# Kernel tuning notes

Hardware: AMD Instinct MI355X
Metric: run time of the kernel (lower is better)

Reference implementation:

```python
import jax, jax.numpy as jnp
import numpy as np

# UnfoldMatmulFold (VOLO outlook attention): kernel_size=3, strides=2, padding=1,
# final_output_shape=(28,28,768). Only valid config per the layer docstring
# (overlap happens exactly once in the fold).
KS, ST, PAD = 3, 2, 1
H, W, C = 28, 28, 768
NH = 12  # num heads (from attn shape)


def setup_inputs() -> dict:
    key = jax.random.key(0)
    k1, k2 = jax.random.split(key)
    B = 64
    hh, ww = 14, 14  # ceil(H/ST), ceil(W/ST)
    vv = jax.random.normal(k1, (B, H, W, C), dtype=jnp.float32)
    attn = jax.random.normal(k2, (B, hh, ww, NH, KS * KS, KS * KS), dtype=jnp.float32)
    return {"vv": vv, "attn": attn}


def _fold_overlap_1(mm):
    # mm: [B, hh, ww, KS, KS, C].  overlap_pad = 2*ST - KS = 1;
    # hh_pad = ww_pad = [0,0] since ceil(28/2)=14 is even.
    aa = jnp.pad(mm, ((0, 0), (0, 0), (0, 0), (0, 1), (0, 1), (0, 0)))  # [B,hh,ww,4,4,C]
    aa = aa.transpose(0, 1, 3, 2, 4, 5)  # [B, hh, 4, ww, 4, C]

    def pad_overlap(p, sh, sw):
        bb = p[:, sh::2, :, sw::2, :, :]  # [B, hh/2, 4, ww/2, 4, C]
        b0, h1, h2, w1, w2, c = bb.shape
        bb = bb.reshape(b0, h1 * h2, w1 * w2, c)  # [B, 28, 28, C]
        ph = (0, ST) if sh == 0 else (ST, 0)
        pw = (0, ST) if sw == 0 else (ST, 0)
        return jnp.pad(bb, ((0, 0), ph, pw, (0, 0)))  # [B, 30, 30, C]

    cc = (pad_overlap(aa, 0, 0) + pad_overlap(aa, 0, 1)
          + pad_overlap(aa, 1, 0) + pad_overlap(aa, 1, 1))
    return cc[:, PAD:PAD + H, PAD:PAD + W, :]  # [B, H, W, C]


def reference(vv, attn):
    B = vv.shape[0]
    hh, ww, nh = attn.shape[1], attn.shape[2], attn.shape[3]
    dh = C // nh
    # unfold (im2col), padding=SAME-style via explicit pad of KS//2
    pad_vv = jnp.pad(vv, ((0, 0), (PAD, PAD), (PAD, PAD), (0, 0)))
    cols = [pad_vv[:, kh:kh + ST * (hh - 1) + 1:ST, kw:kw + ST * (ww - 1) + 1:ST, :]
            for kh in range(KS) for kw in range(KS)]
    patches = jnp.stack(cols, axis=3)  # [B, hh, ww, KS*KS, C], (kh,kw,C) order like tf.extract_patches
    # matmul: per-location per-head attention over the KS*KS window
    v = patches.reshape(B, hh, ww, KS * KS, nh, dh)
    mm = jnp.einsum('bhwnpq,bhwqnd->bhwpnd', attn, v)  # [B,hh,ww,KS*KS,nh,dh]
    mm = mm.reshape(B, hh, ww, KS, KS, C)
    # fold with overlap-add
    return _fold_overlap_1(mm)
```

## Files before the change

kernel.cpp:

```cpp
#include <hip/hip_runtime.h>
#include <stdint.h>

#define HOUT 28
#define HH   14
#define NHEADS 12
#define CC   768
#define NPIX (HOUT * HOUT)
#define NQ   (HH * HH)
#define AHW  (NHEADS * 81)

template<int IO, int JO>
__device__ __forceinline__ void fma9(float4& acc,
                                     const float* __restrict__ ap,
                                     const float4 (&v)[5][5])
{
    #pragma unroll
    for (int qh = 0; qh < 3; ++qh)
        #pragma unroll
        for (int qw = 0; qw < 3; ++qw) {
            const float  a = ap[3 * qh + qw];
            const float4 u = v[IO + qh][JO + qw];
            acc.x = fmaf(a, u.x, acc.x);
            acc.y = fmaf(a, u.y, acc.y);
            acc.z = fmaf(a, u.z, acc.z);
            acc.w = fmaf(a, u.w, acc.w);
        }
}

__global__ __launch_bounds__(192)
void UnfoldMatmulFold_kernel(const float* __restrict__ vv,
                             const float* __restrict__ attn,
                             float* __restrict__ out)
{
    const unsigned id   = blockIdx.x;
    const unsigned xcd  = id & 7u;
    const unsigned g    = id >> 3;
    const unsigned bgrp = g / 28u;
    const unsigned m    = g - bgrp * 28u;
    const int b   = (int)((bgrp << 3) | xcd);
    const int qy  = (int)(m >> 1);
    const int qx0 = (int)((m & 1u) * 7u);
    const int y0  = qy << 1;

    const int tid = threadIdx.x;
    const int c4  = tid << 2;
    const int n   = tid >> 4;

    const float* vb = vv + (size_t)b * (NPIX * CC) + c4;

    const float* vrow[5];
    bool rowok[5];
    #pragma unroll
    for (int i = 0; i < 5; ++i) {
        const int r  = y0 - 1 + i;
        rowok[i]     = ((unsigned)r < HOUT);
        const int rs = rowok[i] ? r : y0;
        vrow[i] = vb + (size_t)(rs * HOUT) * CC;
    }
    const bool hasY = (qy < 13);

    const float* abq = attn + (size_t)b * (NQ * AHW) + n * 81
                     + (size_t)(qy * HH + qx0) * AHW;

    const size_t obrow = (((size_t)b * HOUT + y0) * HOUT) * CC + c4;

    #pragma unroll 1
    for (int t = 0; t < 7; ++t) {
        const int qx = qx0 + t;
        const int x0 = qx << 1;

        float4 v[5][5];
        #pragma unroll
        for (int i = 0; i < 5; ++i) {
            #pragma unroll
            for (int jj = 0; jj < 5; ++jj) {
                const int cpos = x0 - 1 + jj;
                const int cs   = ((unsigned)cpos < HOUT) ? cpos : x0;
                v[i][jj] = *(const float4*)(vrow[i] + (size_t)cs * CC);
            }
        }
        #pragma unroll
        for (int i = 0; i < 5; ++i) {
            #pragma unroll
            for (int jj = 0; jj < 5; ++jj) {
                const bool cv = (unsigned)(x0 - 1 + jj) < HOUT;
                if (!(rowok[i] && cv)) {
                    v[i][jj].x = 0.f; v[i][jj].y = 0.f;
                    v[i][jj].z = 0.f; v[i][jj].w = 0.f;
                }
            }
        }

        const float* a00 = abq + (size_t)t * AHW;
        const float* a01 = a00 + AHW;
        const float* a10 = a00 + (size_t)HH * AHW;
        const float* a11 = a10 + AHW;
        const bool hasX = (qx < 13);

        const size_t ob = obrow + (size_t)x0 * CC;
        float4 acc;

        acc.x = acc.y = acc.z = acc.w = 0.f;
        fma9<0, 0>(acc, a00 + 4 * 9, v);
        *(float4*)&out[ob] = acc;

        acc.x = acc.y = acc.z = acc.w = 0.f;
        fma9<0, 0>(acc, a00 + 5 * 9, v);
        if (hasX) fma9<0, 2>(acc, a01 + 3 * 9, v);
        *(float4*)&out[ob + CC] = acc;

        acc.x = acc.y = acc.z = acc.w = 0.f;
        fma9<0, 0>(acc, a00 + 7 * 9, v);
        if (hasY) fma9<2, 0>(acc, a10 + 1 * 9, v);
        *(float4*)&out[ob + HOUT * CC] = acc;

        acc.x = acc.y = acc.z = acc.w = 0.f;
        fma9<0, 0>(acc, a00 + 8 * 9, v);
        if (hasX) fma9<0, 2>(acc, a01 + 6 * 9, v);
        if (hasY) fma9<2, 0>(acc, a10 + 2 * 9, v);
        if (hasX && hasY) fma9<2, 2>(acc, a11 + 0 * 9, v);
        *(float4*)&out[ob + (HOUT + 1) * CC] = acc;
    }
}

extern "C" void kernel_launch(void* const* d_in, const int* in_sizes, int n_in,
                              void* d_out, int out_size, void* d_ws, size_t ws_size,
                              hipStream_t stream) {
    const float* vv   = (const float*)d_in[0];
    const float* attn = (const float*)d_in[1];
    float* out        = (float*)d_out;

    const int B = in_sizes[0] / (NPIX * CC);
    dim3 grid((unsigned)(B * 28));
    UnfoldMatmulFold_kernel<<<grid, 192, 0, stream>>>(vv, attn, out);
}
```

Before: 350.9 us.

## Stage attention weights in LDS and process two patch columns per block

Each block now handles one pair of adjacent patch positions with 384 threads, replacing the serial 7-step loop per block. The grid grows to B*98 blocks. The six attention neighbourhoods a block needs are staged cooperatively into shared memory, laid out with padded rows so each thread reads its weights as vector loads. Outputs use nontemporal stores. The aim is more parallelism and fewer redundant scattered global reads of attention weights, at the cost of LDS use, a barrier, and repeated halo loads of vv across blocks.

```diff
diff --git a/kernel.cpp b/kernel.cpp
--- a/kernel.cpp
+++ b/kernel.cpp
@@ -9,118 +9,146 @@
 #define NQ   (HH * HH)
 #define AHW  (NHEADS * 81)
 
+#define ALDS_Q  12
+#define ALDS_P  (9 * ALDS_Q)
+#define ALDS_HW (NHEADS * ALDS_P)
+#define ALDS_TOTAL (6 * ALDS_HW)
+
+typedef float vfloat4 __attribute__((ext_vector_type(4)));
+
 template<int IO, int JO>
-__device__ __forceinline__ void fma9(float4& acc,
-                                     const float* __restrict__ ap,
-                                     const float4 (&v)[5][5])
+__device__ __forceinline__ void fma9L(float4& acc,
+                                      const float* ap,
+                                      const float4 (&v)[5][5])
 {
+    const float4 q0 = *(const float4*)(ap + 0);
+    const float4 q1 = *(const float4*)(ap + 4);
+    const float  a8 = ap[8];
+    const float a[9] = {q0.x, q0.y, q0.z, q0.w, q1.x, q1.y, q1.z, q1.w, a8};
     #pragma unroll
     for (int qh = 0; qh < 3; ++qh)
         #pragma unroll
         for (int qw = 0; qw < 3; ++qw) {
-            const float  a = ap[3 * qh + qw];
-            const float4 u = v[IO + qh][JO + qw];
-            acc.x = fmaf(a, u.x, acc.x);
-            acc.y = fmaf(a, u.y, acc.y);
-            acc.z = fmaf(a, u.z, acc.z);
-            acc.w = fmaf(a, u.w, acc.w);
+            const float  aa = a[qh * 3 + qw];
+            const float4 u  = v[IO + qh][JO + qw];
+            acc.x = fmaf(aa, u.x, acc.x);
+            acc.y = fmaf(aa, u.y, acc.y);
+            acc.z = fmaf(aa, u.z, acc.z);
+            acc.w = fmaf(aa, u.w, acc.w);
         }
 }
 
-__global__ __launch_bounds__(192)
+__global__ __launch_bounds__(384, 3)
 void UnfoldMatmulFold_kernel(const float* __restrict__ vv,
                              const float* __restrict__ attn,
                              float* __restrict__ out)
 {
     const unsigned id   = blockIdx.x;
     const unsigned xcd  = id & 7u;
-    const unsigned g    = id >> 3;
-    const unsigned bgrp = g / 28u;
-    const unsigned m    = g - bgrp * 28u;
+    const unsigned j    = id >> 3;
+    const unsigned bgrp = j / 98u;
+    const unsigned pr   = j - bgrp * 98u;
     const int b   = (int)((bgrp << 3) | xcd);
-    const int qy  = (int)(m >> 1);
-    const int qx0 = (int)((m & 1u) * 7u);
+    const int qy  = (int)(pr / 7u);
+    const int qxp = (int)(pr - (unsigned)qy * 7u);
+    const int w0  = qxp << 1;
     const int y0  = qy << 1;
 
-    const int tid = threadIdx.x;
-    const int c4  = tid << 2;
-    const int n   = tid >> 4;
+    const int tid  = threadIdx.x;
+    const int qloc = tid >= 192;
+    const int t    = tid - (qloc ? 192 : 0);
+    const int c4   = t << 2;
+    const int n    = t >> 4;
+    const int qx   = w0 + qloc;
+    const int x0   = qx << 1;
+
+    __shared__ __align__(16) float att_lds[ALDS_TOTAL];
 
     const float* vb = vv + (size_t)b * (NPIX * CC) + c4;
-
-    const float* vrow[5];
+    float4 v[5][5];
     bool rowok[5];
     #pragma unroll
     for (int i = 0; i < 5; ++i) {
         const int r  = y0 - 1 + i;
         rowok[i]     = ((unsigned)r < HOUT);
         const int rs = rowok[i] ? r : y0;
-        vrow[i] = vb + (size_t)(rs * HOUT) * CC;
+        const float* vrow = vb + (size_t)(rs * HOUT) * CC;
+        #pragma unroll
+        for (int jj = 0; jj < 5; ++jj) {
+            const int cpos = x0 - 1 + jj;
+            const int cs   = ((unsigned)cpos < HOUT) ? cpos : x0;
+            v[i][jj] = *(const float4*)(vrow + (size_t)cs * CC);
+        }
     }
-    const bool hasY = (qy < 13);
 
-    const float* abq = attn + (size_t)b * (NQ * AHW) + n * 81
-                     + (size_t)(qy * HH + qx0) * AHW;
-
-    const size_t obrow = (((size_t)b * HOUT + y0) * HOUT) * CC + c4;
-
-    #pragma unroll 1
-    for (int t = 0; t < 7; ++t) {
-        const int qx = qx0 + t;
-        const int x0 = qx << 1;
-
-        float4 v[5][5];
+    {
+        const float* abase = attn + (size_t)b * (NQ * AHW);
         #pragma unroll
-        for (int i = 0; i < 5; ++i) {
+        for (int c = 0; c < 6; ++c) {
+            const int dy = c / 3, dw = c - dy * 3;
+            int h = qy + dy; if (h > 13) h = 13;
+            int w = w0 + dw; if (w > 13) w = 13;
+            const float* g = abase + (size_t)(h * HH + w) * AHW;
+            float* l = att_lds + c * ALDS_HW;
             #pragma unroll
-            for (int jj = 0; jj < 5; ++jj) {
-                const int cpos = x0 - 1 + jj;
-                const int cs   = ((unsigned)cpos < HOUT) ? cpos : x0;
-                v[i][jj] = *(const float4*)(vrow[i] + (size_t)cs * CC);
-            }
-        }
-        #pragma unroll
-        for (int i = 0; i < 5; ++i) {
-            #pragma unroll
-            for (int jj = 0; jj < 5; ++jj) {
-                const bool cv = (unsigned)(x0 - 1 + jj) < HOUT;
-                if (!(rowok[i] && cv)) {
-                    v[i][jj].x = 0.f; v[i][jj].y = 0.f;
-                    v[i][jj].z = 0.f; v[i][jj].w = 0.f;
+            for (int k = 0; k < 3; ++k) {
+                const int inner = tid + k * 384;
+                if (inner < AHW) {
+                    const int nn = inner / 81;
+                    const int r  = inner - nn * 81;
+                    const int p  = r / 9;
+                    const int q  = r - p * 9;
+                    l[nn * ALDS_P + p * ALDS_Q + q] = g[inner];
                 }
             }
         }
+    }
 
-        const float* a00 = abq + (size_t)t * AHW;
-        const float* a01 = a00 + AHW;
-        const float* a10 = a00 + (size_t)HH * AHW;
-        const float* a11 = a10 + AHW;
-        const bool hasX = (qx < 13);
+    #pragma unroll
+    for (int i = 0; i < 5; ++i) {
+        #pragma unroll
+        for (int jj = 0; jj < 5; ++jj) {
+            const bool cv = (unsigned)(x0 - 1 + jj) < HOUT;
+            if (!(rowok[i] && cv)) {
+                v[i][jj].x = 0.f; v[i][jj].y = 0.f;
+                v[i][jj].z = 0.f; v[i][jj].w = 0.f;
+            }
+        }
+    }
 
-        const size_t ob = obrow + (size_t)x0 * CC;
-        float4 acc;
+    __syncthreads();
 
-        acc.x = acc.y = acc.z = acc.w = 0.f;
-        fma9<0, 0>(acc, a00 + 4 * 9, v);
-        *(float4*)&out[ob] = acc;
+    const float* A00 = att_lds + (0 + qloc    ) * ALDS_HW + n * ALDS_P;
+    const float* A01 = att_lds + (0 + qloc + 1) * ALDS_HW + n * ALDS_P;
+    const float* A10 = att_lds + (3 + qloc    ) * ALDS_HW + n * ALDS_P;
+    const float* A11 = att_lds + (3 + qloc + 1) * ALDS_HW + n * ALDS_P;
 
-        acc.x = acc.y = acc.z = acc.w = 0.f;
-        fma9<0, 0>(acc, a00 + 5 * 9, v);
-        if (hasX) fma9<0, 2>(acc, a01 + 3 * 9, v);
-        *(float4*)&out[ob + CC] = acc;
+    const bool hasX = (qx < 13);
+    const bool hasY = (qy < 13);
 
-        acc.x = acc.y = acc.z = acc.w = 0.f;
-        fma9<0, 0>(acc, a00 + 7 * 9, v);
-        if (hasY) fma9<2, 0>(acc, a10 + 1 * 9, v);
-        *(float4*)&out[ob + HOUT * CC] = acc;
+    const size_t ob = (((size_t)b * HOUT + y0) * HOUT + x0) * CC + c4;
+    float4 acc;
 
-        acc.x = acc.y = acc.z = acc.w = 0.f;
-        fma9<0, 0>(acc, a00 + 8 * 9, v);
-        if (hasX) fma9<0, 2>(acc, a01 + 6 * 9, v);
-        if (hasY) fma9<2, 0>(acc, a10 + 2 * 9, v);
-        if (hasX && hasY) fma9<2, 2>(acc, a11 + 0 * 9, v);
-        *(float4*)&out[ob + (HOUT + 1) * CC] = acc;
-    }
+    acc.x = acc.y = acc.z = acc.w = 0.f;
+    fma9L<0, 0>(acc, A00 + 4 * ALDS_Q, v);
+    __builtin_nontemporal_store(*(vfloat4*)&acc, (vfloat4*)&out[ob]);
+
+    acc.x = acc.y = acc.z = acc.w = 0.f;
+    fma9L<0, 0>(acc, A00 + 5 * ALDS_Q, v);
+    if (hasX) fma9L<0, 2>(acc, A01 + 3 * ALDS_Q, v);
+    __builtin_nontemporal_store(*(vfloat4*)&acc, (vfloat4*)&out[ob + CC]);
+
+    acc.x = acc.y = acc.z = acc.w = 0.f;
+    fma9L<0, 0>(acc, A00 + 7 * ALDS_Q, v);
+    if (hasY) fma9L<2, 0>(acc, A10 + 1 * ALDS_Q, v);
+    __builtin_nontemporal_store(*(vfloat4*)&acc, (vfloat4*)&out[ob + HOUT * CC]);
+
+    acc.x = acc.y = acc.z = acc.w = 0.f;
+    fma9L<0, 0>(acc, A00 + 8 * ALDS_Q, v);
+    if (hasX) fma9L<0, 2>(acc, A01 + 6 * ALDS_Q, v);
+    if (hasY) fma9L<2, 0>(acc, A10 + 2 * ALDS_Q, v);
+    if (hasX && hasY) fma9L<2, 2>(acc, A11 + 0 * ALDS_Q, v);
+    __builtin_nontemporal_store(*(vfloat4*)&acc, (vfloat4*)&out[ob + (HOUT + 1) * CC]);
 }
 
 extern "C" void kernel_launch(void* const* d_in, const int* in_sizes, int n_in,
@@ -131,6 +159,6 @@
     float* out        = (float*)d_out;
 
     const int B = in_sizes[0] / (NPIX * CC);
-    dim3 grid((unsigned)(B * 28));
-    UnfoldMatmulFold_kernel<<<grid, 192, 0, stream>>>(vv, attn, out);
+    dim3 grid((unsigned)(B * 98));
+    UnfoldMatmulFold_kernel<<<grid, 384, 0, stream>>>(vv, attn, out);
 }
```

New measurement: 377.9 us. +7.7%, slower.
